# Kernel optimization log

Measured on AMD Instinct MI355X. Metric: run time of the kernel, lower is better.

Reference implementation:

```python
import jax, jax.numpy as jnp
import numpy as np
from jax import lax

# ---- config (matches DecodePredictions init kwargs) ----
MAX_PER_CLASS = 100
MAX_TOTAL = 100
IOU_THRESH = 0.5
SCORE_THRESH = 0.05
NUM_CLASSES = 80
K_CAND = 512  # per-class candidate pool kept before NMS (bounds the O(K^2) IoU work)
BOX_VARIANCE = np.array([0.1, 0.1, 0.2, 0.2], np.float32)


def generate_anchors(height, width):
    """RetinaNet anchors (keras.io AnchorBox): FPN levels 3-7, 3 ratios x 3 scales, [cx,cy,w,h] in pixels."""
    ratios = [0.5, 1.0, 2.0]
    scales = [2 ** 0.0, 2 ** (1.0 / 3.0), 2 ** (2.0 / 3.0)]
    all_anchors = []
    for level in range(3, 8):
        stride = 2 ** level
        area = float((2 ** (level + 2)) ** 2)  # 32^2 .. 512^2
        dims = []
        for r in ratios:
            ah = np.sqrt(area / r)
            aw = area / ah
            for s in scales:
                dims.append([s * aw, s * ah])
        dims = np.asarray(dims, np.float32)  # [9, 2] = (w, h)
        fh = int(np.ceil(height / stride))
        fw = int(np.ceil(width / stride))
        rx = (np.arange(fw, dtype=np.float32) + 0.5) * stride
        ry = (np.arange(fh, dtype=np.float32) + 0.5) * stride
        cx, cy = np.meshgrid(rx, ry)
        centers = np.stack([cx, cy], -1)[:, :, None, :].repeat(9, axis=2)  # [fh,fw,9,2]
        d = np.broadcast_to(dims, (fh, fw, 9, 2))
        all_anchors.append(np.concatenate([centers, d], -1).reshape(-1, 4).astype(np.float32))
    return jnp.asarray(np.concatenate(all_anchors, 0))  # [N, 4]


def _pairwise_iou(b):
    # Generic TF NMS IoU formula treating coords as [y1,x1,y2,x2] (module feeds cx,cy,w,h -- replicated faithfully).
    y1, x1, y2, x2 = b[:, 0], b[:, 1], b[:, 2], b[:, 3]
    area = jnp.maximum(y2 - y1, 0.0) * jnp.maximum(x2 - x1, 0.0)
    ih = jnp.maximum(jnp.minimum(y2[:, None], y2[None, :]) - jnp.maximum(y1[:, None], y1[None, :]), 0.0)
    iw = jnp.maximum(jnp.minimum(x2[:, None], x2[None, :]) - jnp.maximum(x1[:, None], x1[None, :]), 0.0)
    inter = ih * iw
    union = area[:, None] + area[None, :] - inter
    return jnp.where(union > 0.0, inter / union, 0.0)


def _nms_single_class(boxes, scores):  # boxes [N,4], scores [N]
    top_s, idx = lax.top_k(scores, K_CAND)          # sort-by-score candidate pool
    top_b = boxes[idx]                               # [K,4]
    keep0 = top_s > SCORE_THRESH                     # score_threshold filter
    iou = _pairwise_iou(top_b)                       # [K,K]
    rng = jnp.arange(K_CAND)

    def body(i, keep):
        sup = (iou[i] > IOU_THRESH) & (rng > i)      # boxes ranked below i suppressed by i
        return jnp.where(keep[i], keep & ~sup, keep)

    keep = lax.fori_loop(0, K_CAND, body, keep0)
    kept_s = jnp.where(keep, top_s, 0.0)
    sel_s, sel = lax.top_k(kept_s, MAX_PER_CLASS)    # max_output_size_per_class
    return top_b[sel], sel_s                         # [P,4], [P]


def _combine(cls_boxes, cls_scores):  # [C,P,4], [C,P] -> combined top MAX_TOTAL for one image
    C, P = cls_scores.shape
    flat_s = cls_scores.reshape(-1)
    flat_b = cls_boxes.reshape(-1, 4)
    flat_c = jnp.repeat(jnp.arange(C, dtype=jnp.float32), P)
    top_s, idx = lax.top_k(flat_s, MAX_TOTAL)
    valid = (top_s > 0.0)
    vf = valid.astype(flat_b.dtype)
    boxes = jnp.clip(flat_b[idx], 0.0, 1.0) * vf[:, None]  # clip_boxes=True, zero-pad invalid
    scores = top_s * vf
    classes = jnp.where(valid, flat_c[idx], 0.0)
    return boxes, scores, classes, valid.sum().astype(jnp.int32)


def _forward(inputs, predictions):
    H, W = inputs.shape[1], inputs.shape[2]
    anchors = generate_anchors(float(H), float(W))            # [N,4] cx,cy,w,h
    cls_scores = jax.nn.sigmoid(predictions[..., :-4])        # [B,N,C]
    box_pred = predictions[..., -4:] * jnp.asarray(BOX_VARIANCE)
    xy = box_pred[..., :2] * anchors[..., 2:] + anchors[..., :2]
    wh = jnp.exp(box_pred[..., 2:]) * anchors[..., 2:]
    boxes = jnp.concatenate([xy, wh], -1)                     # [B,N,4] decoded

    per_class = jax.vmap(jax.vmap(_nms_single_class, in_axes=(None, 1)), in_axes=(0, 0))
    cb, cs = per_class(boxes, cls_scores)                     # [B,C,P,4], [B,C,P]
    return jax.vmap(_combine)(cb, cs)                         # boxes, scores, classes, valid


def setup_inputs() -> dict:
    key = jax.random.key(0)
    k1, k2 = jax.random.split(key)
    inputs = jax.random.uniform(k1, (4, 640, 640, 3), jnp.float32)
    predictions = jax.random.normal(k2, (4, 76725, NUM_CLASSES + 4), jnp.float32)
    return {"inputs": inputs, "predictions": predictions}


def reference(inputs, predictions):
    return _forward(inputs, predictions)
```

## Files before the change

kernel.cpp:

```cpp
#include <hip/hip_runtime.h>
#include <cmath>

#define NA 76725
#define NCLS 80
#define NB 4
#define KC 512
#define MPC 100
#define MT 100
#define TT 256
#define NTILE 300
#define NSLOTP 300
#define PADN 76800
#define NCAND 1024
#define SLOT 16
#define SPLIT 8
#define THRESH_LOGIT 2.3f

struct Dims { float d[5 * 9 * 2]; };


__device__ __forceinline__ unsigned keyof(float x) {
    unsigned u = __float_as_uint(x);
    return u ^ ((u & 0x80000000u) ? 0xFFFFFFFFu : 0x80000000u);
}
__device__ __forceinline__ float unkey(unsigned k) {
    unsigned u = (k & 0x80000000u) ? (k ^ 0x80000000u) : ~k;
    return __uint_as_float(u);
}
__device__ __forceinline__ float sigmoidf_dev(float x) {
    if (x >= 0.f) return 1.f / (1.f + expf(-x));
    float e = expf(x);
    return e / (1.f + e);
}
__device__ __forceinline__ unsigned long long compose(unsigned key, int a) {
    return ((unsigned long long)key << 32) | (unsigned long long)(0xFFFFFFFFu - (unsigned)a);
}

__device__ __forceinline__ float4 decode_box(float4 p, int a, const Dims& dims) {
    const int base[5] = {0, 57600, 72000, 75600, 76500};
    const int fw[5] = {80, 40, 20, 10, 5};
    const float strd[5] = {8.f, 16.f, 32.f, 64.f, 128.f};
    int l;
    if (a < 57600) l = 0;
    else if (a < 72000) l = 1;
    else if (a < 75600) l = 2;
    else if (a < 76500) l = 3;
    else l = 4;
    int i = a - base[l];
    int cell = i / 9, k = i - cell * 9;
    int x = cell % fw[l], y = cell / fw[l];
    float cx = ((float)x + 0.5f) * strd[l];
    float cy = ((float)y + 0.5f) * strd[l];
    float aw = dims.d[(l * 9 + k) * 2 + 0];
    float ah = dims.d[(l * 9 + k) * 2 + 1];
    float bx = __fmul_rn(p.x, 0.1f), by = __fmul_rn(p.y, 0.1f);
    float bw = __fmul_rn(p.z, 0.2f), bh = __fmul_rn(p.w, 0.2f);
    float4 o;
    o.x = __fadd_rn(__fmul_rn(bx, aw), cx);
    o.y = __fadd_rn(__fmul_rn(by, ah), cy);
    o.z = __fmul_rn(expf(bw), aw);
    o.w = __fmul_rn(expf(bh), ah);
    return o;
}


__global__ __launch_bounds__(256) void scan_kernel(const float* __restrict__ pred,
                                                   unsigned long long* __restrict__ candbuf,
                                                   int* __restrict__ counts2) {
    __shared__ int cnt[NCLS];
    const int blk = blockIdx.x;
    const int b = blk / NTILE, tix = blk - b * NTILE;
    const int t0 = tix * TT;
    int nrow = NA - t0; if (nrow > TT) nrow = TT;

    if (threadIdx.x < NCLS) cnt[threadIdx.x] = 0;
    __syncthreads();

    const float4* src = reinterpret_cast<const float4*>(pred + ((size_t)b * NA + t0) * 84);
    const int nv = nrow * 21;
    unsigned long long* slotbase = candbuf + ((size_t)(b * NCLS) * NSLOTP + tix) * SLOT;
    for (int i = threadIdx.x; i < nv; i += 256) {
        const float4 v = src[i];
        const int row = i / 21, chunk = i - row * 21;
        if (chunk == 20) continue;
        const int a = t0 + row, cbase = chunk * 4;
        const float vals[4] = {v.x, v.y, v.z, v.w};
        #pragma unroll
        for (int q = 0; q < 4; ++q) {
            if (vals[q] > THRESH_LOGIT) {
                const int c = cbase + q;
                const int p = atomicAdd(&cnt[c], 1);
                if (p < SLOT)
                    slotbase[(size_t)c * NSLOTP * SLOT + p] = compose(keyof(vals[q]), a);
            }
        }
    }
    __syncthreads();
    if (threadIdx.x < NCLS)
        counts2[(size_t)(b * NCLS + threadIdx.x) * NSLOTP + tix] = cnt[threadIdx.x];
}


__device__ __forceinline__ void find_bin(int* hist, int bins, int remaining,
                                         int* sh3, int* wsum) {
    const int tid = threadIdx.x;
    const int lane = tid & 63, wv = tid >> 6;
    const int nit = (bins + 511) >> 9;
    int lsum = 0;
    for (int q = 0; q < nit; ++q) {
        int rr = tid * nit + q;
        if (rr < bins) lsum += hist[bins - 1 - rr];
    }
    int acc = lsum;
    #pragma unroll
    for (int off = 1; off < 64; off <<= 1) {
        int x = __shfl_up(acc, off);
        if (lane >= off) acc += x;
    }
    if (lane == 63) wsum[wv] = acc;
    __syncthreads();
    int base = 0;
    for (int w = 0; w < wv; ++w) base += wsum[w];
    int run = base + acc - lsum;
    for (int q = 0; q < nit; ++q) {
        int rr = tid * nit + q;
        if (rr < bins) {
            int h = hist[bins - 1 - rr];
            if (run < remaining && remaining <= run + h) { sh3[0] = bins - 1 - rr; sh3[1] = run; sh3[2] = h; }
            run += h;
        }
    }
    __syncthreads();
}


__global__ __launch_bounds__(512) void topk2_kernel(const float* __restrict__ pred,
                                                    const unsigned long long* __restrict__ candbuf,
                                                    const int* __restrict__ counts2,
                                                    float* __restrict__ top_score,
                                                    float4* __restrict__ sel_boxes, Dims dims) {
    const int col = blockIdx.x;
    const int b = col / NCLS, cc = col - b * NCLS;
    const int tid = threadIdx.x;
    const int lane = tid & 63, wv = tid >> 6;

    __shared__ int hist4k[4096];
    __shared__ unsigned long long buf[KC];
    __shared__ int hist[256];
    __shared__ int sh3[3];
    __shared__ int wsum[8];
    __shared__ int gcount, eqtaken, totsh, ovfsh;
    __shared__ int wcnt[8];
    unsigned long long* cand = (unsigned long long*)hist4k;
    int* scnt = hist4k + 2048;
    int* spfx = hist4k + 2560;

    if (tid == 0) { totsh = 0; ovfsh = 0; }
    int lsum = (tid < NSLOTP) ? counts2[(size_t)col * NSLOTP + tid] : 0;
    scnt[tid] = lsum;
    if (lsum > SLOT) ovfsh = 1;
    int acc = lsum;
    #pragma unroll
    for (int off = 1; off < 64; off <<= 1) {
        int x = __shfl_up(acc, off);
        if (lane >= off) acc += x;
    }
    if (lane == 63) wsum[wv] = acc;
    __syncthreads();
    int base = 0;
    for (int w = 0; w < wv; ++w) base += wsum[w];
    spfx[tid] = base + acc - lsum;
    if (tid == 511) totsh = base + acc;
    __syncthreads();

    const int tot = totsh;
    const bool fastok = (!ovfsh) && tot >= KC && tot <= NCAND;
    int mode = 0;

    if (fastok) {
        cand[tid] = 0ull; cand[tid + 512] = 0ull;
        __syncthreads();
        const unsigned long long* src = candbuf + (size_t)col * NSLOTP * SLOT;
        for (int i = tid; i < NSLOTP * SLOT; i += 512) {
            const int e = i >> 4, q = i & (SLOT - 1);
            const unsigned long long v = src[i];
            if (q < scnt[e]) cand[spfx[e] + q] = v;
        }
        __syncthreads();
    } else {
        const float* colp = pred + (size_t)b * NA * 84 + cc;
        for (int i = tid; i < 4096; i += 512) hist4k[i] = 0;
        __syncthreads();
        for (int a = tid; a < NA; a += 512)
            atomicAdd(&hist4k[keyof(colp[(size_t)a * 84]) >> 20], 1);
        __syncthreads();
        find_bin(hist4k, 4096, KC, sh3, wsum);
        const int bsel = sh3[0], above = sh3[1], ceq1 = sh3[2];
        const int ncand = above + ceq1;

        if (ncand <= NCAND) {
            const unsigned fk = ((unsigned)bsel) << 20;
            if (tid == 0) gcount = 0;
            cand[tid] = 0ull; cand[tid + 512] = 0ull;
            __syncthreads();
            for (int a = tid; a < NA; a += 512) {
                unsigned k = keyof(colp[(size_t)a * 84]);
                if (k >= fk) { int p = atomicAdd(&gcount, 1); cand[p] = compose(k, a); }
            }
            __syncthreads();
        } else {
            mode = 1;
            unsigned prefix = ((unsigned)bsel) << 20;
            int remaining = KC - above;

            for (int i = tid; i < 4096; i += 512) hist4k[i] = 0;
            __syncthreads();
            for (int a = tid; a < NA; a += 512) {
                unsigned k = keyof(colp[(size_t)a * 84]);
                if ((k & 0xFFF00000u) == prefix) atomicAdd(&hist4k[(k >> 8) & 4095], 1);
            }
            __syncthreads();
            find_bin(hist4k, 4096, remaining, sh3, wsum);
            prefix |= ((unsigned)sh3[0]) << 8;
            remaining -= sh3[1];

            if (tid < 256) hist[tid] = 0;
            __syncthreads();
            for (int a = tid; a < NA; a += 512) {
                unsigned k = keyof(colp[(size_t)a * 84]);
                if ((k & 0xFFFFFF00u) == prefix) atomicAdd(&hist[k & 255], 1);
            }
            __syncthreads();
            find_bin(hist, 256, remaining, sh3, wsum);
            prefix |= (unsigned)sh3[0];
            remaining -= sh3[1];

            const unsigned K = prefix;
            const int cgt = KC - remaining;
            const int need = remaining;
            if (tid == 0) { gcount = 0; eqtaken = 0; }
            __syncthreads();
            for (int bs = 0; bs < PADN; bs += 512) {
                int a = bs + tid;
                unsigned key = (a < NA) ? keyof(colp[(size_t)a * 84]) : 0u;
                if (a < NA && key > K) {
                    int p = atomicAdd(&gcount, 1);
                    buf[p] = compose(key, a);
                }
                bool eq = (key == K) && (a < NA);
                unsigned long long m = __ballot(eq);
                if (lane == 0) wcnt[wv] = __popcll(m);
                __syncthreads();
                int off = eqtaken;
                for (int w = 0; w < wv; ++w) off += wcnt[w];
                int rank = off + __popcll(m & ((1ull << lane) - 1ull));
                if (eq && rank < need)
                    buf[cgt + rank] = compose(K, a);
                __syncthreads();
                if (tid == 0) {
                    int s = 0;
                    for (int w = 0; w < 8; ++w) s += wcnt[w];
                    eqtaken += s;
                }
                __syncthreads();
            }
        }
    }

    if (mode == 0) {
        for (int k2 = 2; k2 <= NCAND; k2 <<= 1) {
            for (int j = k2 >> 1; j > 0; j >>= 1) {
                __syncthreads();
                for (int i = tid; i < NCAND; i += 512) {
                    int ixj = i ^ j;
                    if (ixj > i) {
                        unsigned long long A = cand[i], B = cand[ixj];
                        bool up = (i & k2) == 0;
                        if (up ? (A < B) : (A > B)) { cand[i] = B; cand[ixj] = A; }
                    }
                }
            }
        }
    } else {
        for (int k2 = 2; k2 <= KC; k2 <<= 1) {
            for (int j = k2 >> 1; j > 0; j >>= 1) {
                __syncthreads();
                {
                    int i = tid, ixj = i ^ j;
                    if (ixj > i) {
                        unsigned long long A = buf[i], B = buf[ixj];
                        bool up = (i & k2) == 0;
                        if (up ? (A < B) : (A > B)) { buf[i] = B; buf[ixj] = A; }
                    }
                }
            }
        }
    }
    __syncthreads();

    {
        const unsigned long long v = (mode == 0) ? cand[tid] : buf[tid];
        const unsigned key = (unsigned)(v >> 32);
        const int a = (int)(0xFFFFFFFFu - (unsigned)(v & 0xFFFFFFFFu));
        top_score[col * KC + tid] = sigmoidf_dev(unkey(key));
        const float4 p4 = *reinterpret_cast<const float4*>(pred + ((size_t)b * NA + a) * 84 + 80);
        sel_boxes[(size_t)col * KC + tid] = decode_box(p4, a, dims);
    }
}


__global__ __launch_bounds__(512) void nms_build_kernel(const float4* __restrict__ sel_boxes,
                                                        unsigned long long* __restrict__ maskbuf) {
    const int blk = blockIdx.x;
    const int col = blk >> 3, part = blk & 7;
    const int tid = threadIdx.x, wave = tid >> 6, lane = tid & 63;
    __shared__ float y1[KC], x1[KC], y2[KC], x2[KC], ar[KC];

    for (int t = tid; t < KC; t += 512) {
        float4 bx = sel_boxes[(size_t)col * KC + t];
        y1[t] = bx.x; x1[t] = bx.y; y2[t] = bx.z; x2[t] = bx.w;
        ar[t] = __fmul_rn(fmaxf(__fsub_rn(bx.z, bx.x), 0.f),
                          fmaxf(__fsub_rn(bx.w, bx.y), 0.f));
    }
    __syncthreads();

    float jy1[8], jx1[8], jy2[8], jx2[8], jar[8];
    #pragma unroll
    for (int w = 0; w < 8; ++w) {
        int j = (w << 6) + lane;
        jy1[w] = y1[j]; jx1[w] = x1[j]; jy2[w] = y2[j]; jx2[w] = x2[j]; jar[w] = ar[j];
    }

    for (int k = 0; k < 8; ++k) {
        const int i = part + SPLIT * (wave + 8 * k);
        const float iy1 = y1[i], ix1 = x1[i], iy2 = y2[i], ix2 = x2[i], iar = ar[i];
        unsigned long long row[8];
        #pragma unroll
        for (int w = 0; w < 8; ++w) {
            unsigned long long m = 0ull;
            if (((w << 6) + 63) > i) {
                const int j = (w << 6) + lane;
                float ih = fmaxf(__fsub_rn(fminf(iy2, jy2[w]), fmaxf(iy1, jy1[w])), 0.f);
                float iw = fmaxf(__fsub_rn(fminf(ix2, jx2[w]), fmaxf(ix1, jx1[w])), 0.f);
                float inter = __fmul_rn(ih, iw);
                float uni = __fsub_rn(__fadd_rn(iar, jar[w]), inter);
                m = __ballot((uni > 0.f) && (inter > __fmul_rn(0.5f, uni)) && (j > i));
            }
            row[w] = m;
        }
        unsigned long long v = row[0];
        v = (lane == 1) ? row[1] : v;
        v = (lane == 2) ? row[2] : v;
        v = (lane == 3) ? row[3] : v;
        v = (lane == 4) ? row[4] : v;
        v = (lane == 5) ? row[5] : v;
        v = (lane == 6) ? row[6] : v;
        v = (lane == 7) ? row[7] : v;
        if (lane < 8) maskbuf[((size_t)col * KC + i) * 8 + lane] = v;
    }
}


__global__ __launch_bounds__(256) void nms_resolve_kernel(const float4* __restrict__ sel_boxes,
                                                          const float* __restrict__ top_score,
                                                          const unsigned long long* __restrict__ maskbuf,
                                                          float4* __restrict__ col_boxes,
                                                          float* __restrict__ col_scores) {
    const int col = blockIdx.x;
    const int tid = threadIdx.x, wv = tid >> 6, lane = tid & 63;
    __shared__ unsigned long long mask[KC * 8];
    __shared__ float y1[KC], x1[KC], y2[KC], x2[KC], sc[KC];
    __shared__ unsigned long long keep0w[8], keepw[8];
    __shared__ int wordpfx[9];
    __shared__ int sel[MPC];

    {
        const unsigned long long* src = maskbuf + (size_t)col * KC * 8;
        for (int m = tid; m < KC * 8; m += 256) mask[m] = src[m];
    }
    for (int t = tid; t < KC; t += 256) {
        float4 bx = sel_boxes[(size_t)col * KC + t];
        y1[t] = bx.x; x1[t] = bx.y; y2[t] = bx.z; x2[t] = bx.w;
        const float s = top_score[col * KC + t];
        sc[t] = s;
        const unsigned long long m = __ballot(s > 0.05f);
        if (lane == 0) keep0w[t >> 6] = m;
    }
    __syncthreads();

    if (wv == 0) {
        const int w8 = lane & 7;
        const unsigned long long kww = keep0w[w8];
        unsigned long long remw = 0ull;
        for (int ib = 0; ib < KC; ib += 8) {
            unsigned long long rows[8];
            #pragma unroll
            for (int u = 0; u < 8; ++u) rows[u] = mask[(ib + u) * 8 + w8];
            #pragma unroll
            for (int u = 0; u < 8; ++u) {
                const int i = ib + u, W = i >> 6, t = i & 63;
                const unsigned long long remW = __shfl(remw, W);
                const unsigned long long kwW = __shfl(kww, W);
                if (((kwW >> t) & 1ull) && !((remW >> t) & 1ull)) remw |= rows[u];
            }
        }
        if (lane < 8) keepw[w8] = kww & ~remw;
    }
    __syncthreads();
    if (tid == 0) {
        int s = 0;
        #pragma unroll
        for (int w = 0; w < 8; ++w) { wordpfx[w] = s; s += __popcll(keepw[w]); }
        wordpfx[8] = s;
    }
    __syncthreads();

    const int nkept = wordpfx[8];
    for (int t = tid; t < KC; t += 256) {
        const unsigned long long w = keepw[t >> 6];
        const int l = t & 63;
        const bool kp = (w >> l) & 1ull;
        const int kb = wordpfx[t >> 6] + __popcll(w & ((1ull << l) - 1ull));
        if (kp) {
            if (kb < MPC) sel[kb] = t;
        } else {
            const int nb = t - kb;
            if (nkept + nb < MPC) sel[nkept + nb] = t;
        }
    }
    __syncthreads();
    if (tid < MPC) {
        int t = sel[tid];
        bool kp = (keepw[t >> 6] >> (t & 63)) & 1ull;
        col_scores[col * MPC + tid] = kp ? sc[t] : 0.f;
        col_boxes[col * MPC + tid] = make_float4(y1[t], x1[t], y2[t], x2[t]);
    }
}


__global__ __launch_bounds__(1024) void combine_kernel(const float4* __restrict__ col_boxes,
                                                       const float* __restrict__ col_scores,
                                                       float* __restrict__ out) {
    const int b = blockIdx.x, tid = threadIdx.x;
    const int wv = tid >> 6, lane = tid & 63;
    __shared__ int hist[256];
    __shared__ unsigned long long cand[128];
    __shared__ int sh3[3];
    __shared__ int gcnt, eqtaken;
    __shared__ int wcnt[16];
    __shared__ int wsc[16];

    const int NTOT = NCLS * MPC;
    unsigned sck[8];
    #pragma unroll
    for (int q = 0; q < 8; ++q) {
        const int t = (q << 10) + tid;
        sck[q] = (t < NTOT) ? __float_as_uint(col_scores[b * NTOT + t]) : 0u;
    }

    unsigned prefix = 0;
    int remaining = MT, ceq = 0;
    #pragma unroll 1
    for (int pass = 0; pass < 4; ++pass) {
        const int shift = 24 - 8 * pass;
        const unsigned mdone = pass ? (0xFFFFFFFFu << (shift + 8)) : 0u;
        if (tid < 256) hist[tid] = 0;
        __syncthreads();
        #pragma unroll
        for (int q = 0; q < 8; ++q) {
            const int t = (q << 10) + tid;
            if (t < NTOT && (sck[q] & mdone) == prefix)
                atomicAdd(&hist[(sck[q] >> shift) & 255], 1);
        }
        __syncthreads();
        int lsum = (tid < 256) ? hist[255 - tid] : 0;
        int acc2 = lsum;
        #pragma unroll
        for (int off = 1; off < 64; off <<= 1) {
            int x = __shfl_up(acc2, off);
            if (lane >= off) acc2 += x;
        }
        if (lane == 63) wsc[wv] = acc2;
        __syncthreads();
        int base2 = 0;
        for (int w = 0; w < wv; ++w) base2 += wsc[w];
        int run = base2 + acc2 - lsum;
        if (tid < 256 && run < remaining && remaining <= run + lsum) { sh3[0] = 255 - tid; sh3[1] = run; sh3[2] = lsum; }
        __syncthreads();
        prefix |= ((unsigned)sh3[0]) << shift;
        remaining -= sh3[1];
        ceq = sh3[2];
        __syncthreads();
    }
    const unsigned S = prefix;
    const int cgt = MT - remaining;

    if (tid == 0) { gcnt = 0; eqtaken = 0; }
    if (tid < 128) cand[tid] = 0ull;
    __syncthreads();
    #pragma unroll
    for (int q = 0; q < 8; ++q) {
        const int t = (q << 10) + tid;
        if (t < NTOT && sck[q] > S) {
            int p = atomicAdd(&gcnt, 1);
            cand[p] = ((unsigned long long)sck[q] << 32) |
                      (unsigned long long)(0xFFFFFFFFu - (unsigned)t);
        }
    }
    __syncthreads();

    if (ceq == remaining) {
        #pragma unroll
        for (int q = 0; q < 8; ++q) {
            const int t = (q << 10) + tid;
            if (t < NTOT && sck[q] == S) {
                int p = atomicAdd(&eqtaken, 1);
                cand[cgt + p] = ((unsigned long long)S << 32) |
                                (unsigned long long)(0xFFFFFFFFu - (unsigned)t);
            }
        }
        __syncthreads();
    } else {
        #pragma unroll 1
        for (int q = 0; q < 8; ++q) {
            const int t = (q << 10) + tid;
            const bool eq = (t < NTOT) && (sck[q] == S);
            unsigned long long m = __ballot(eq);
            if (lane == 0) wcnt[wv] = __popcll(m);
            __syncthreads();
            int off = eqtaken;
            for (int w = 0; w < wv; ++w) off += wcnt[w];
            int rank = off + __popcll(m & ((1ull << lane) - 1ull));
            if (eq && rank < remaining)
                cand[cgt + rank] = ((unsigned long long)S << 32) |
                                   (unsigned long long)(0xFFFFFFFFu - (unsigned)t);
            __syncthreads();
            if (tid == 0) {
                int s = 0;
                for (int w = 0; w < 16; ++w) s += wcnt[w];
                eqtaken += s;
            }
            __syncthreads();
        }
    }

    for (int k2 = 2; k2 <= 128; k2 <<= 1) {
        for (int j = k2 >> 1; j > 0; j >>= 1) {
            __syncthreads();
            if (tid < 128) {
                int i = tid, ixj = i ^ j;
                if (ixj > i) {
                    unsigned long long A = cand[i], B = cand[ixj];
                    bool up = (i & k2) == 0;
                    if (up ? (A < B) : (A > B)) { cand[i] = B; cand[ixj] = A; }
                }
            }
        }
    }
    __syncthreads();
    if (tid == 0) gcnt = 0;
    __syncthreads();
    if (tid < MT) {
        unsigned long long v = cand[tid];
        float s = __uint_as_float((unsigned)(v >> 32));
        int f = (int)(0xFFFFFFFFu - (unsigned)(v & 0xFFFFFFFFu));
        bool valid = (s > 0.f);
        int cl = 0, p = 0;
        float4 bx = make_float4(0.f, 0.f, 0.f, 0.f);
        if (valid) {
            cl = f / MPC;
            p = f - cl * MPC;
            float4 raw = col_boxes[((size_t)b * NCLS + cl) * MPC + p];
            bx.x = fminf(fmaxf(raw.x, 0.f), 1.f);
            bx.y = fminf(fmaxf(raw.y, 0.f), 1.f);
            bx.z = fminf(fmaxf(raw.z, 0.f), 1.f);
            bx.w = fminf(fmaxf(raw.w, 0.f), 1.f);
            atomicAdd(&gcnt, 1);
        }
        int o = b * MT + tid;
        out[o * 4 + 0] = bx.x;
        out[o * 4 + 1] = bx.y;
        out[o * 4 + 2] = bx.z;
        out[o * 4 + 3] = bx.w;
        out[NB * MT * 4 + o] = valid ? s : 0.f;
        out[NB * MT * 5 + o] = valid ? (float)cl : 0.f;
    }
    __syncthreads();
    if (tid == 0) out[NB * MT * 6 + b] = (float)gcnt;
}


extern "C" void kernel_launch(void* const* d_in, const int* in_sizes, int n_in,
                              void* d_out, int out_size, void* d_ws, size_t ws_size,
                              hipStream_t stream) {
    const float* pred = (const float*)d_in[1];
    float* out = (float*)d_out;
    char* ws = (char*)d_ws;

    Dims dims;
    const double ratios[3] = {0.5, 1.0, 2.0};
    for (int l = 0; l < 5; ++l) {
        double side = (double)(1 << (l + 5));
        double area = side * side;
        for (int ri = 0; ri < 3; ++ri) {
            double ah = sqrt(area / ratios[ri]);
            double aw = area / ah;
            for (int si = 0; si < 3; ++si) {
                double s = pow(2.0, (double)si / 3.0);
                dims.d[(l * 9 + ri * 3 + si) * 2 + 0] = (float)(s * aw);
                dims.d[(l * 9 + ri * 3 + si) * 2 + 1] = (float)(s * ah);
            }
        }
    }

    const size_t SZ_CAND = (size_t)NB * NCLS * NSLOTP * SLOT * 8;
    const size_t SZ_CNT  = (size_t)NB * NCLS * NSLOTP * 4;
    const size_t SZ_SC   = (size_t)NB * NCLS * KC * 4;
    const size_t SZ_SEL  = (size_t)NB * NCLS * KC * 16;
    const size_t SZ_CB   = (size_t)NB * NCLS * MPC * 16;

    unsigned long long* candbuf    = (unsigned long long*)(ws);
    int*                counts2    = (int*)(ws + SZ_CAND);
    float*              top_score  = (float*)(ws + SZ_CAND + SZ_CNT);
    float4*             sel_boxes  = (float4*)(ws + SZ_CAND + SZ_CNT + SZ_SC);
    float4*             col_boxes  = (float4*)(ws + SZ_CAND + SZ_CNT + SZ_SC + SZ_SEL);
    float*              col_scores = (float*)(ws + SZ_CAND + SZ_CNT + SZ_SC + SZ_SEL + SZ_CB);
    unsigned long long* maskbuf    = (unsigned long long*)(ws);

    scan_kernel<<<NB * NTILE, 256, 0, stream>>>(pred, candbuf, counts2);
    topk2_kernel<<<NB * NCLS, 512, 0, stream>>>(pred, candbuf, counts2, top_score, sel_boxes, dims);
    nms_build_kernel<<<NB * NCLS * SPLIT, 512, 0, stream>>>(sel_boxes, maskbuf);
    nms_resolve_kernel<<<NB * NCLS, 256, 0, stream>>>(sel_boxes, top_score, maskbuf, col_boxes, col_scores);
    combine_kernel<<<NB, 1024, 0, stream>>>(col_boxes, col_scores, out);
}
```

Measured before the change: 304.6 us.

## Stage scan hits in LDS, unroll loads, widen NMS resolve blocks

The scan kernel now buffers candidate hits in shared memory and writes only the valid slots to global memory in a single coalesced pass, instead of scattering stores from inside the atomic path. Its main loop issues four float4 loads per iteration so more memory requests are in flight. The NMS resolve kernel moves to 512 threads, so each thread handles exactly one candidate. This adds 10KB of LDS per scan block, which may reduce occupancy.

```diff
diff --git a/kernel.cpp b/kernel.cpp
--- a/kernel.cpp
+++ b/kernel.cpp
@@ -68,6 +68,7 @@
                                                    unsigned long long* __restrict__ candbuf,
                                                    int* __restrict__ counts2) {
     __shared__ int cnt[NCLS];
+    __shared__ unsigned long long hitbuf[NCLS * SLOT];
     const int blk = blockIdx.x;
     const int b = blk / NTILE, tix = blk - b * NTILE;
     const int t0 = tix * TT;
@@ -78,24 +79,44 @@
 
     const float4* src = reinterpret_cast<const float4*>(pred + ((size_t)b * NA + t0) * 84);
     const int nv = nrow * 21;
-    unsigned long long* slotbase = candbuf + ((size_t)(b * NCLS) * NSLOTP + tix) * SLOT;
-    for (int i = threadIdx.x; i < nv; i += 256) {
+
+    #define PROC(v, idx) do {                                                  \
+        const int row_ = (idx) / 21, chunk_ = (idx) - row_ * 21;               \
+        if (chunk_ != 20) {                                                    \
+            const int a_ = t0 + row_, cbase_ = chunk_ * 4;                     \
+            const float vals_[4] = {(v).x, (v).y, (v).z, (v).w};               \
+            _Pragma("unroll")                                                  \
+            for (int q_ = 0; q_ < 4; ++q_) {                                   \
+                if (vals_[q_] > THRESH_LOGIT) {                                \
+                    const int c_ = cbase_ + q_;                                \
+                    const int p_ = atomicAdd(&cnt[c_], 1);                     \
+                    if (p_ < SLOT)                                             \
+                        hitbuf[c_ * SLOT + p_] = compose(keyof(vals_[q_]), a_);\
+                }                                                              \
+            }                                                                  \
+        }                                                                      \
+    } while (0)
+
+    int i = threadIdx.x;
+    for (; i + 768 < nv; i += 1024) {
+        const float4 v0 = src[i];
+        const float4 v1 = src[i + 256];
+        const float4 v2 = src[i + 512];
+        const float4 v3 = src[i + 768];
+        PROC(v0, i); PROC(v1, i + 256); PROC(v2, i + 512); PROC(v3, i + 768);
+    }
+    for (; i < nv; i += 256) {
         const float4 v = src[i];
-        const int row = i / 21, chunk = i - row * 21;
-        if (chunk == 20) continue;
-        const int a = t0 + row, cbase = chunk * 4;
-        const float vals[4] = {v.x, v.y, v.z, v.w};
-        #pragma unroll
-        for (int q = 0; q < 4; ++q) {
-            if (vals[q] > THRESH_LOGIT) {
-                const int c = cbase + q;
-                const int p = atomicAdd(&cnt[c], 1);
-                if (p < SLOT)
-                    slotbase[(size_t)c * NSLOTP * SLOT + p] = compose(keyof(vals[q]), a);
-            }
-        }
-    }
-    __syncthreads();
+        PROC(v, i);
+    }
+    #undef PROC
+    __syncthreads();
+
+    for (int e = threadIdx.x; e < NCLS * SLOT; e += 256) {
+        const int c = e >> 4, q = e & (SLOT - 1);
+        if (q < cnt[c])
+            candbuf[(((size_t)(b * NCLS + c)) * NSLOTP + tix) * SLOT + q] = hitbuf[e];
+    }
     if (threadIdx.x < NCLS)
         counts2[(size_t)(b * NCLS + threadIdx.x) * NSLOTP + tix] = cnt[threadIdx.x];
 }
@@ -361,7 +382,7 @@
 }
 
 
-__global__ __launch_bounds__(256) void nms_resolve_kernel(const float4* __restrict__ sel_boxes,
+__global__ __launch_bounds__(512) void nms_resolve_kernel(const float4* __restrict__ sel_boxes,
                                                           const float* __restrict__ top_score,
                                                           const unsigned long long* __restrict__ maskbuf,
                                                           float4* __restrict__ col_boxes,
@@ -376,9 +397,10 @@
 
     {
         const unsigned long long* src = maskbuf + (size_t)col * KC * 8;
-        for (int m = tid; m < KC * 8; m += 256) mask[m] = src[m];
-    }
-    for (int t = tid; t < KC; t += 256) {
+        for (int m = tid; m < KC * 8; m += 512) mask[m] = src[m];
+    }
+    {
+        const int t = tid;
         float4 bx = sel_boxes[(size_t)col * KC + t];
         y1[t] = bx.x; x1[t] = bx.y; y2[t] = bx.z; x2[t] = bx.w;
         const float s = top_score[col * KC + t];
@@ -416,7 +438,8 @@
     __syncthreads();
 
     const int nkept = wordpfx[8];
-    for (int t = tid; t < KC; t += 256) {
+    {
+        const int t = tid;
         const unsigned long long w = keepw[t >> 6];
         const int l = t & 63;
         const bool kp = (w >> l) & 1ull;
@@ -630,6 +653,6 @@
     scan_kernel<<<NB * NTILE, 256, 0, stream>>>(pred, candbuf, counts2);
     topk2_kernel<<<NB * NCLS, 512, 0, stream>>>(pred, candbuf, counts2, top_score, sel_boxes, dims);
     nms_build_kernel<<<NB * NCLS * SPLIT, 512, 0, stream>>>(sel_boxes, maskbuf);
-    nms_resolve_kernel<<<NB * NCLS, 256, 0, stream>>>(sel_boxes, top_score, maskbuf, col_boxes, col_scores);
+    nms_resolve_kernel<<<NB * NCLS, 512, 0, stream>>>(sel_boxes, top_score, maskbuf, col_boxes, col_scores);
     combine_kernel<<<NB, 1024, 0, stream>>>(col_boxes, col_scores, out);
 }
```

Measured after the change: 297.8 us. 2.2% less time.
